# Performance work log

Hardware: AMD Instinct MI355X
Metric: run time of the kernel (lower is better)

The kernel has to match this reference:

```python
import jax, jax.numpy as jnp
import numpy as np

NUM_HEADS = 16
NUM_KV_HEADS = 8
HEAD_DIM = 128
HIDDEN = 2048
Q_SIZE = NUM_HEADS * HEAD_DIM          # 2048
KV_SIZE = NUM_KV_HEADS * HEAD_DIM      # 1024
SCALING = 256.0 ** -0.5                # query_pre_attn_scalar ** -0.5
EPS = 1e-6
BATCH = 8
ENC_LEN = 512                          # encoder_len_per_req
Q_LEN = 2048                           # sum of extend_seq_lens (8 * 256)
KV_LEN = BATCH * ENC_LEN               # 4096


def _rms_norm(x, w):
    # Gemma3RMSNorm: fp32 compute, scale by (1 + weight)
    xf = x.astype(jnp.float32)
    xf = xf * jax.lax.rsqrt(jnp.mean(xf * xf, axis=-1, keepdims=True) + EPS)
    return (xf * (1.0 + w.astype(jnp.float32))).astype(x.dtype)


def setup_inputs() -> dict:
    key = jax.random.key(0)
    k1, k2, k3 = jax.random.split(key, 3)
    return {
        "hidden_states": jax.random.normal(k1, (Q_LEN, HIDDEN), jnp.float32),
        "encoder_hidden_states": jax.random.normal(k2, (KV_LEN, HIDDEN), jnp.float32),
        "w_qkv": jax.random.normal(k3, (Q_SIZE + 2 * KV_SIZE, HIDDEN), jnp.float32) * 0.02,
        "q_norm_w": jnp.zeros((HEAD_DIM,), jnp.float32),
        "k_norm_w": jnp.zeros((HEAD_DIM,), jnp.float32),
        "seq_lens": jnp.full((BATCH,), Q_LEN // BATCH, jnp.int32),  # extend_seq_lens per request
    }


def reference(hidden_states, encoder_hidden_states, w_qkv, q_norm_w, k_norm_w, seq_lens):
    # decoder side: only q is used
    qkv_dec = hidden_states @ w_qkv.T                     # [q_len, 4096]
    q = qkv_dec[:, :Q_SIZE].reshape(Q_LEN, NUM_HEADS, HEAD_DIM)
    q = _rms_norm(q, q_norm_w) * SCALING

    # encoder side: only k, v are used
    qkv_enc = encoder_hidden_states @ w_qkv.T             # [kv_len, 4096]
    k = qkv_enc[:, Q_SIZE:Q_SIZE + KV_SIZE].reshape(KV_LEN, NUM_KV_HEADS, HEAD_DIM)
    v = qkv_enc[:, Q_SIZE + KV_SIZE:].reshape(KV_LEN, NUM_KV_HEADS, HEAD_DIM)
    k = _rms_norm(k, k_norm_w)

    # GQA: repeat each kv head n_rep times (consecutively, matching expand+reshape)
    n_rep = NUM_HEADS // NUM_KV_HEADS
    k = jnp.repeat(k, n_rep, axis=1)                      # [kv_len, H, D]
    v = jnp.repeat(v, n_rep, axis=1)

    # scores per head: [H, q_len, kv_len]
    scores = jnp.einsum('qhd,khd->hqk', q, k)

    # ragged block-diagonal mask: query token i belongs to request r iff
    # cumsum(seq_lens)[r-1] <= i < cumsum(seq_lens)[r]; kv token j -> j // ENC_LEN
    q_req = jnp.searchsorted(jnp.cumsum(seq_lens), jnp.arange(Q_LEN), side='right')
    kv_req = jnp.arange(KV_LEN) // ENC_LEN
    mask = q_req[:, None] == kv_req[None, :]              # [q_len, kv_len] bool
    scores = jnp.where(mask[None, :, :], scores, -jnp.inf)

    attn = jax.nn.softmax(scores.astype(jnp.float32), axis=-1).astype(v.dtype)
    out = jnp.einsum('hqk,khd->qhd', attn, v)             # [q_len, H, D]
    return out.reshape(Q_LEN, NUM_HEADS * HEAD_DIM)
```

## Files before the change

kernel.cpp:

```cpp
#include <hip/hip_runtime.h>

typedef __attribute__((ext_vector_type(8))) short short8;
typedef __attribute__((ext_vector_type(4))) float f32x4;

#define DEVI __device__ __forceinline__

static constexpr int HIDDEN   = 2048;
static constexpr int NHEADS   = 16;
static constexpr int NKV      = 8;
static constexpr int HDIM     = 128;
static constexpr int QLEN     = 2048;
static constexpr int KVLEN    = 4096;
static constexpr int ENCLEN   = 512;
static constexpr int NREQ     = 8;
static constexpr float SCALING = 0.0625f;
static constexpr float EPS     = 1e-6f;

DEVI unsigned short f2bf(float f) {
  unsigned int b = __float_as_uint(f);
  b += 0x7FFFu + ((b >> 16) & 1u);
  return (unsigned short)(b >> 16);
}

DEVI void g2l16(const void* g, void* l) {
  __builtin_amdgcn_global_load_lds(
      (const __attribute__((address_space(1))) void*)g,
      (__attribute__((address_space(3))) void*)l, 16, 0, 0);
}

__global__ __launch_bounds__(256) void cvt_all(const float* __restrict__ h,
                                               const float* __restrict__ e,
                                               const float* __restrict__ w,
                                               unsigned short* __restrict__ hb,
                                               unsigned short* __restrict__ eb,
                                               unsigned short* __restrict__ wb) {
  constexpr long S1 = (long)2048 * 2048, S2 = (long)4096 * 2048;
  long i = ((long)blockIdx.x * 256 + threadIdx.x) * 8;
  const float* src;
  unsigned short* dst;
  if (i < S1)           { src = h + i;            dst = hb + i; }
  else if (i < S1 + S2) { src = e + (i - S1);     dst = eb + (i - S1); }
  else                  { src = w + (i - S1 - S2); dst = wb + (i - S1 - S2); }
  float4 a = *(const float4*)src;
  float4 b = *(const float4*)(src + 4);
  short8 o;
  o[0] = (short)f2bf(a.x); o[1] = (short)f2bf(a.y);
  o[2] = (short)f2bf(a.z); o[3] = (short)f2bf(a.w);
  o[4] = (short)f2bf(b.x); o[5] = (short)f2bf(b.y);
  o[6] = (short)f2bf(b.z); o[7] = (short)f2bf(b.w);
  *(short8*)dst = o;
}


#define SBAR  __builtin_amdgcn_s_barrier()

DEVI short8 rdfrag(const char* half, int row, int g) {
  return *(const short8*)(half + row * 128 + ((g ^ (row & 7)) << 4));
}

__global__ __launch_bounds__(512, 2) void gemm_qkv8(
    const unsigned short* __restrict__ Adec, const unsigned short* __restrict__ Aenc,
    const unsigned short* __restrict__ Bw,
    const float* __restrict__ q_nw, const float* __restrict__ k_nw,
    unsigned short* __restrict__ q_bf, unsigned short* __restrict__ k_bf,
    unsigned short* __restrict__ v_t) {
  extern __shared__ char lds[];
  const int K = 2048, NKT = 32;

  int flat = blockIdx.y * 8 + blockIdx.x;
  int swz = (flat & 7) * 24 + (flat >> 3);
  int bx = swz & 7, by = swz >> 3;

  const unsigned short* A;
  int bm0;
  if (by < 8) { A = Adec; bm0 = by * 256; }
  else        { A = Aenc; bm0 = (by - 8) * 256; }
  const unsigned short* Bp = Bw + (by < 8 ? 0 : (size_t)2048 * 2048);
  const int bn0 = bx * 256;

  const int tid = threadIdx.x, lane = tid & 63, wave = tid >> 6;
  const int lr = lane & 15, lg = lane >> 4;
  const int wr = wave >> 2, wc = wave & 3;
  const int bcol0 = (wc & 1) * 64;

#define AH(b, h) (lds + (b) * 65536 + (h) * 16384)
#define BH(b, h) (lds + (b) * 65536 + 32768 + (h) * 16384)

  int srow[2], scol[2];
#pragma unroll
  for (int i = 0; i < 2; ++i) {
    int c = i * 512 + tid;
    srow[i] = c >> 3;
    scol[i] = ((c & 7) ^ ((c >> 3) & 7)) * 8;
  }

#define STG_KT(kt)                                                            \
  {                                                                           \
    const int b_ = (kt) & 1;                                                  \
    const size_t kb_ = (size_t)(kt) * 64;                                     \
    _Pragma("unroll") for (int i = 0; i < 2; ++i) {                           \
      const int d_ = (i * 512 + tid) * 16;                                    \
      g2l16(A  + (size_t)(bm0 + srow[i]) * K + kb_ + scol[i],       AH(b_, 0) + d_); \
      g2l16(A  + (size_t)(bm0 + 128 + srow[i]) * K + kb_ + scol[i], AH(b_, 1) + d_); \
      g2l16(Bp + (size_t)(bn0 + srow[i]) * K + kb_ + scol[i],       BH(b_, 0) + d_); \
      g2l16(Bp + (size_t)(bn0 + 128 + srow[i]) * K + kb_ + scol[i], BH(b_, 1) + d_); \
    }                                                                         \
  }

  f32x4 acc[8][4] = {};
  short8 a[4][2], b[2][2];

#define LOAD_A(buf, qm)                                                       \
  {                                                                           \
    const char* ah = AH(buf, wr);                                             \
    _Pragma("unroll") for (int m = 0; m < 4; ++m)                             \
        _Pragma("unroll") for (int kk = 0; kk < 2; ++kk)                      \
            a[m][kk] = rdfrag(ah, (qm) * 64 + m * 16 + lr, kk * 4 + lg);      \
  }
#define LOAD_B(buf, qn)                                                       \
  {                                                                           \
    const char* bh = BH(buf, wc >> 1);                                        \
    _Pragma("unroll") for (int n = 0; n < 2; ++n)                             \
        _Pragma("unroll") for (int kk = 0; kk < 2; ++kk)                      \
            b[n][kk] = rdfrag(bh, bcol0 + (qn) * 32 + n * 16 + lr, kk * 4 + lg); \
  }
#define MM16(qm, qn)                                                          \
  {                                                                           \
    __builtin_amdgcn_s_setprio(1);                                            \
    _Pragma("unroll") for (int m = 0; m < 4; ++m)                             \
        _Pragma("unroll") for (int n = 0; n < 2; ++n)                         \
            _Pragma("unroll") for (int kk = 0; kk < 2; ++kk)                  \
                acc[(qm)*4 + m][(qn)*2 + n] =                                 \
                    __builtin_amdgcn_mfma_f32_16x16x32_bf16(                  \
                        a[m][kk], b[n][kk], acc[(qm)*4 + m][(qn)*2 + n], 0, 0, 0); \
    __builtin_amdgcn_s_setprio(0);                                            \
  }

  STG_KT(0);
  asm volatile("s_waitcnt vmcnt(0)" ::: "memory");
  SBAR;

#pragma unroll 2
  for (int kt = 0; kt < NKT; ++kt) {
    const int cb = kt & 1;
    if (kt + 1 < NKT) STG_KT(kt + 1);
    LOAD_A(cb, 0); LOAD_B(cb, 0); SBAR; MM16(0, 0); SBAR;
    LOAD_B(cb, 1);                SBAR; MM16(0, 1); SBAR;
    LOAD_A(cb, 1); LOAD_B(cb, 0); SBAR; MM16(1, 0); SBAR;
    LOAD_B(cb, 1);                SBAR; MM16(1, 1);
    if (kt + 1 < NKT) asm volatile("s_waitcnt vmcnt(0)" ::: "memory");
    SBAR;
  }

  const int btype = (by < 8) ? 0 : (bx < 4 ? 1 : 2);
  const int tokbase0 = (by < 8 ? by : by - 8) * 256;

  if (btype < 2) {
    float* Lf = (float*)lds;
    const float* wnorm = (btype == 0) ? q_nw : k_nw;
    const float fscale = (btype == 0) ? SCALING : 1.0f;
    unsigned short* dst = (btype == 0) ? q_bf : k_bf;
    const size_t LEN = (btype == 0) ? (size_t)QLEN : (size_t)KVLEN;
    const int dloc = lr * 8;
    float wv[8];
#pragma unroll
    for (int j = 0; j < 8; ++j) wv[j] = 1.0f + wnorm[dloc + j];

#pragma unroll
    for (int q = 0; q < 4; ++q) {
      SBAR;
      if (wr == (q >> 1)) {
        const int amb = (q & 1) * 4;
#pragma unroll
        for (int am2 = 0; am2 < 4; ++am2)
#pragma unroll
          for (int n = 0; n < 4; ++n)
#pragma unroll
            for (int r = 0; r < 4; ++r)
              Lf[(am2 * 16 + lg * 4 + r) * 260 + wc * 64 + n * 16 + lr] =
                  acc[amb + am2][n][r];
      }
      SBAR;
#pragma unroll
      for (int it = 0; it < 4; ++it) {
        int pair = it * 32 + wave * 4 + (lane >> 4);
        int row = pair >> 1, hh = pair & 1;
        const float* src = &Lf[row * 260 + hh * 128 + dloc];
        f32x4 x0 = *(const f32x4*)src;
        f32x4 x1 = *(const f32x4*)(src + 4);
        float ssq = x0[0]*x0[0] + x0[1]*x0[1] + x0[2]*x0[2] + x0[3]*x0[3] +
                    x1[0]*x1[0] + x1[1]*x1[1] + x1[2]*x1[2] + x1[3]*x1[3];
#pragma unroll
        for (int m = 8; m >= 1; m >>= 1) ssq += __shfl_xor(ssq, m);
        float sc = rsqrtf(ssq * (1.0f / 128.0f) + EPS) * fscale;
        short8 o;
        o[0] = (short)f2bf(x0[0] * sc * wv[0]); o[1] = (short)f2bf(x0[1] * sc * wv[1]);
        o[2] = (short)f2bf(x0[2] * sc * wv[2]); o[3] = (short)f2bf(x0[3] * sc * wv[3]);
        o[4] = (short)f2bf(x1[0] * sc * wv[4]); o[5] = (short)f2bf(x1[1] * sc * wv[5]);
        o[6] = (short)f2bf(x1[2] * sc * wv[6]); o[7] = (short)f2bf(x1[3] * sc * wv[7]);
        int tok = tokbase0 + q * 64 + row;
        int hd = 2 * bx + hh;
        *(short8*)&dst[((size_t)hd * LEN + tok) * 128 + dloc] = o;
      }
    }
  } else {
    float* Lv = (float*)lds;
#pragma unroll
    for (int q = 0; q < 4; ++q) {
      SBAR;
      if (wr == (q >> 1)) {
        const int amb = (q & 1) * 4;
#pragma unroll
        for (int am2 = 0; am2 < 4; ++am2)
#pragma unroll
          for (int n = 0; n < 4; ++n)
            *(f32x4*)&Lv[(wc * 64 + n * 16 + lr) * 68 + am2 * 16 + lg * 4] =
                acc[amb + am2][n];
      }
      SBAR;
      int d = tid >> 1, th = tid & 1;
      const float* src = &Lv[d * 68 + th * 32];
      int kh = (bx - 4) * 2 + (d >> 7);
      int tok = tokbase0 + q * 64 + th * 32;
      unsigned short* vp = &v_t[((size_t)kh * 128 + (d & 127)) * KVLEN + tok];
#pragma unroll
      for (int j = 0; j < 4; ++j) {
        f32x4 v0 = *(const f32x4*)(src + j * 8);
        f32x4 v1 = *(const f32x4*)(src + j * 8 + 4);
        short8 o;
        o[0] = (short)f2bf(v0[0]); o[1] = (short)f2bf(v0[1]);
        o[2] = (short)f2bf(v0[2]); o[3] = (short)f2bf(v0[3]);
        o[4] = (short)f2bf(v1[0]); o[5] = (short)f2bf(v1[1]);
        o[6] = (short)f2bf(v1[2]); o[7] = (short)f2bf(v1[3]);
        *(short8*)(vp + j * 8) = o;
      }
    }
  }
#undef AH
#undef BH
#undef STG_KT
#undef LOAD_A
#undef LOAD_B
#undef MM16
}

__global__ __launch_bounds__(256, 4) void attn_kernel(
    const unsigned short* __restrict__ qb,
    const unsigned short* __restrict__ kb,
    const unsigned short* __restrict__ vt,
    const int* __restrict__ seq_lens,
    float* __restrict__ out) {
  __shared__ __align__(16) char smem[73728];

  const int h = blockIdx.y;
  const int t0 = blockIdx.x * 64;
  int req = 0, qs = 0;
#pragma unroll 1
  while (req < NREQ - 1 && qs + seq_lens[req] <= t0) { qs += seq_lens[req]; ++req; }
  const int slen = seq_lens[req];
  const int rows = min(64, qs + slen - t0);
  if (rows <= 0) return;
  const int qbase = t0;

  const int tid = threadIdx.x, lane = tid & 63, wave = tid >> 6;
  const int lr = lane & 15, lg = lane >> 4;
  const int m0w = wave * 16;
  const int kh = h >> 1;
  const int kv0 = req * ENCLEN;

#define STAGE_K(c, db)                                                        \
  _Pragma("unroll") for (int i = 0; i < 4; ++i) {                             \
    int idx = i * 256 + tid;                                                  \
    int row = idx >> 4, slot = idx & 15;                                      \
    g2l16(kb + ((size_t)kh * KVLEN + kv0 + (c) * 64 + row) * 128 +            \
              ((slot ^ (row & 15)) << 3),                                     \
          smem + (db) * 16384 + idx * 16);                                    \
  }
#define STAGE_V(c, db)                                                        \
  _Pragma("unroll") for (int i = 0; i < 4; ++i) {                             \
    int idx = i * 256 + tid;                                                  \
    int row = idx >> 3, slot = idx & 7;                                       \
    g2l16(vt + ((size_t)kh * 128 + row) * KVLEN + kv0 + (c) * 64 +            \
              ((slot ^ (row & 7)) << 3),                                      \
          smem + 32768 + (db) * 16384 + idx * 16);                            \
  }

  unsigned short* Ps = (unsigned short*)(smem + 65536);

  short8 a_q[4];
  {
    int qr = qbase + min(m0w + lr, rows - 1);
    const unsigned short* qp = qb + ((size_t)h * QLEN + qr) * 128 + lg * 8;
#pragma unroll
    for (int ks = 0; ks < 4; ++ks) a_q[ks] = *(const short8*)(qp + ks * 32);
  }

  f32x4 acc[8] = {};
  float mrow[4], lsum[4];
#pragma unroll
  for (int r = 0; r < 4; ++r) { mrow[r] = -1e30f; lsum[r] = 0.f; }

  STAGE_K(0, 0); STAGE_V(0, 0);

  int cb = 0;
#pragma unroll 1
  for (int c = 0; c < 8; ++c) {
    asm volatile("s_waitcnt vmcnt(0)" ::: "memory");
    __syncthreads();
    if (c < 7) { STAGE_K(c + 1, cb ^ 1); STAGE_V(c + 1, cb ^ 1); }
    const unsigned short* Kb = (const unsigned short*)(smem + cb * 16384);
    const unsigned short* Vb = (const unsigned short*)(smem + 32768 + cb * 16384);

    f32x4 s[4] = {};
#pragma unroll
    for (int ks = 0; ks < 4; ++ks) {
      short8 bk[4];
#pragma unroll
      for (int n = 0; n < 4; ++n) {
        int row = n * 16 + lr;
        bk[n] = *(const short8*)&Kb[row * 128 + (((ks * 4 + lg) ^ (row & 15)) << 3)];
      }
#pragma unroll
      for (int n = 0; n < 4; ++n)
        s[n] = __builtin_amdgcn_mfma_f32_16x16x32_bf16(a_q[ks], bk[n], s[n], 0, 0, 0);
    }

#pragma unroll
    for (int r = 0; r < 4; ++r) {
      float mx = fmaxf(fmaxf(s[0][r], s[1][r]), fmaxf(s[2][r], s[3][r]));
#pragma unroll
      for (int msk = 8; msk >= 1; msk >>= 1) mx = fmaxf(mx, __shfl_xor(mx, msk));
      float mnew = fmaxf(mrow[r], mx);
      float al = __expf(mrow[r] - mnew);
      mrow[r] = mnew;
      float rs = 0.f;
#pragma unroll
      for (int n = 0; n < 4; ++n) {
        float p = __expf(s[n][r] - mnew);
        s[n][r] = p;
        rs += p;
      }
#pragma unroll
      for (int msk = 8; msk >= 1; msk >>= 1) rs += __shfl_xor(rs, msk);
      lsum[r] = lsum[r] * al + rs;
#pragma unroll
      for (int n2 = 0; n2 < 8; ++n2) acc[n2][r] *= al;
    }

#pragma unroll
    for (int n = 0; n < 4; ++n)
#pragma unroll
      for (int r = 0; r < 4; ++r) {
        int row = m0w + lg * 4 + r;
        int col = n * 16 + lr;
        Ps[row * 64 + (col ^ ((row & 7) << 3))] = f2bf(s[n][r]);
      }
    asm volatile("s_waitcnt lgkmcnt(0)" ::: "memory");
    __builtin_amdgcn_sched_barrier(0);

#pragma unroll
    for (int ks = 0; ks < 2; ++ks) {
      int prow = m0w + lr;
      short8 pa = *(const short8*)&Ps[prow * 64 + (((ks * 4 + lg) ^ (prow & 7)) << 3)];
#pragma unroll
      for (int n2 = 0; n2 < 8; ++n2) {
        int row = n2 * 16 + lr;
        short8 bv = *(const short8*)&Vb[row * 64 + (((ks * 4 + lg) ^ (row & 7)) << 3)];
        acc[n2] = __builtin_amdgcn_mfma_f32_16x16x32_bf16(pa, bv, acc[n2], 0, 0, 0);
      }
    }
    cb ^= 1;
  }
  __syncthreads();

  float inv[4];
#pragma unroll
  for (int r = 0; r < 4; ++r) inv[r] = 1.0f / lsum[r];
#pragma unroll
  for (int n2 = 0; n2 < 8; ++n2)
#pragma unroll
    for (int r = 0; r < 4; ++r) acc[n2][r] *= inv[r];

  constexpr int OFS = 132;
  float* Of = (float*)smem;
#pragma unroll
  for (int n2 = 0; n2 < 8; ++n2)
#pragma unroll
    for (int r = 0; r < 4; ++r)
      Of[(m0w + lg * 4 + r) * OFS + n2 * 16 + lr] = acc[n2][r];
  __syncthreads();
#pragma unroll
  for (int p = 0; p < 8; ++p) {
    int idx = p * 256 + tid;
    int row = idx >> 5, c4 = (idx & 31) * 4;
    if (row < rows) {
      f32x4 v = *(const f32x4*)&Of[row * OFS + c4];
      *(f32x4*)&out[(size_t)(qbase + row) * 2048 + h * 128 + c4] = v;
    }
  }
#undef STAGE_K
#undef STAGE_V
}

extern "C" void kernel_launch(void* const* d_in, const int* in_sizes, int n_in,
                              void* d_out, int out_size, void* d_ws, size_t ws_size,
                              hipStream_t stream) {
  const float* hidden = (const float*)d_in[0];
  const float* enc    = (const float*)d_in[1];
  const float* w_qkv  = (const float*)d_in[2];
  const float* q_nw   = (const float*)d_in[3];
  const float* k_nw   = (const float*)d_in[4];
  const int*   slens  = (const int*)d_in[5];
  float* out = (float*)d_out;

  char* ws = (char*)d_ws;
  unsigned short* h_bf = (unsigned short*)(ws + 0);
  unsigned short* e_bf = (unsigned short*)(ws + 8388608);
  unsigned short* w_bf = (unsigned short*)(ws + 25165824);
  unsigned short* q_bf = (unsigned short*)(ws + 41943040);
  unsigned short* k_bf = (unsigned short*)(ws + 50331648);
  unsigned short* v_t  = (unsigned short*)(ws + 58720256);

  static bool attr_set = false;
  if (!attr_set) {
    hipFuncSetAttribute((const void*)gemm_qkv8,
                        hipFuncAttributeMaxDynamicSharedMemorySize, 131072);
    attr_set = true;
  }

  cvt_all<<<10240, 256, 0, stream>>>(hidden, enc, w_qkv, h_bf, e_bf, w_bf);

  gemm_qkv8<<<dim3(8, 24), 512, 131072, stream>>>(h_bf, e_bf, w_bf, q_nw, k_nw,
                                                  q_bf, k_bf, v_t);

  attn_kernel<<<dim3(32, 16), 256, 0, stream>>>(q_bf, k_bf, v_t, slens, out);
}
```

Before: 114.4 us.

## Interleave half-tile global staging with MFMA phases in QKV GEMM main loop

The QKV projection GEMM main loop is restructured. Global-to-LDS staging is split into half-tile A and B chunks, spread across four compute phases per k-tile, and B is prefetched one tile further ahead than A. Each wave now loads its B fragments once per k-tile and its A fragments per quarter, and waits on global loads with a partial vmcnt instead of draining fully each iteration. The goal is to overlap memory traffic with MFMA work and cut full-drain stalls, at the cost of more barriers and more complex hand scheduling.

```diff
diff --git a/kernel.cpp b/kernel.cpp
--- a/kernel.cpp
+++ b/kernel.cpp
@@ -65,7 +65,7 @@
     unsigned short* __restrict__ q_bf, unsigned short* __restrict__ k_bf,
     unsigned short* __restrict__ v_t) {
   extern __shared__ char lds[];
-  const int K = 2048, NKT = 32;
+  const int K = 2048;
 
   int flat = blockIdx.y * 8 + blockIdx.x;
   int swz = (flat & 7) * 24 + (flat >> 3);
@@ -81,75 +81,87 @@
   const int tid = threadIdx.x, lane = tid & 63, wave = tid >> 6;
   const int lr = lane & 15, lg = lane >> 4;
   const int wr = wave >> 2, wc = wave & 3;
-  const int bcol0 = (wc & 1) * 64;
-
-#define AH(b, h) (lds + (b) * 65536 + (h) * 16384)
-#define BH(b, h) (lds + (b) * 65536 + 32768 + (h) * 16384)
 
   int srow[2], scol[2];
 #pragma unroll
-  for (int i = 0; i < 2; ++i) {
-    int c = i * 512 + tid;
-    srow[i] = c >> 3;
-    scol[i] = ((c & 7) ^ ((c >> 3) & 7)) * 8;
-  }
-
-#define STG_KT(kt)                                                            \
-  {                                                                           \
-    const int b_ = (kt) & 1;                                                  \
-    const size_t kb_ = (size_t)(kt) * 64;                                     \
-    _Pragma("unroll") for (int i = 0; i < 2; ++i) {                           \
-      const int d_ = (i * 512 + tid) * 16;                                    \
-      g2l16(A  + (size_t)(bm0 + srow[i]) * K + kb_ + scol[i],       AH(b_, 0) + d_); \
-      g2l16(A  + (size_t)(bm0 + 128 + srow[i]) * K + kb_ + scol[i], AH(b_, 1) + d_); \
-      g2l16(Bp + (size_t)(bn0 + srow[i]) * K + kb_ + scol[i],       BH(b_, 0) + d_); \
-      g2l16(Bp + (size_t)(bn0 + 128 + srow[i]) * K + kb_ + scol[i], BH(b_, 1) + d_); \
-    }                                                                         \
-  }
+  for (int i2 = 0; i2 < 2; ++i2) {
+    int c = i2 * 512 + tid;
+    srow[i2] = c >> 3;
+    scol[i2] = ((c & 7) ^ ((c >> 3) & 7)) * 8;
+  }
+
+#define STGH_A(kt, h)                                                         \
+  { _Pragma("unroll") for (int i2 = 0; i2 < 2; ++i2)                          \
+      g2l16(A + (size_t)(bm0 + (h) * 128 + srow[i2]) * K + (size_t)(kt) * 64 + scol[i2], \
+            lds + (((kt) & 1) << 16) + ((h) << 14) + (i2 * 512 + tid) * 16); }
+#define STGH_B(kt, h)                                                         \
+  { _Pragma("unroll") for (int i2 = 0; i2 < 2; ++i2)                          \
+      g2l16(Bp + (size_t)(bn0 + (h) * 128 + srow[i2]) * K + (size_t)(kt) * 64 + scol[i2], \
+            lds + (((kt) & 1) << 16) + 32768 + ((h) << 14) + (i2 * 512 + tid) * 16); }
 
   f32x4 acc[8][4] = {};
-  short8 a[4][2], b[2][2];
-
-#define LOAD_A(buf, qm)                                                       \
-  {                                                                           \
-    const char* ah = AH(buf, wr);                                             \
-    _Pragma("unroll") for (int m = 0; m < 4; ++m)                             \
+  short8 a[2][2], b[4][2];
+
+#define RDB(buf)                                                              \
+  { const char* bh = lds + ((buf) << 16) + 32768 + ((wc >> 1) << 14);         \
+    _Pragma("unroll") for (int n = 0; n < 4; ++n)                             \
+      _Pragma("unroll") for (int kk = 0; kk < 2; ++kk)                        \
+        b[n][kk] = rdfrag(bh, (wc & 1) * 64 + n * 16 + lr, kk * 4 + lg); }
+#define RDA(buf, q)                                                           \
+  { const char* ah = lds + ((buf) << 16) + (wr << 14);                        \
+    _Pragma("unroll") for (int j = 0; j < 2; ++j)                             \
+      _Pragma("unroll") for (int kk = 0; kk < 2; ++kk)                        \
+        a[j][kk] = rdfrag(ah, ((q) * 2 + j) * 16 + lr, kk * 4 + lg); }
+#define MM16(q)                                                               \
+  { __builtin_amdgcn_s_setprio(1);                                            \
+    _Pragma("unroll") for (int j = 0; j < 2; ++j)                             \
+      _Pragma("unroll") for (int n = 0; n < 4; ++n)                           \
         _Pragma("unroll") for (int kk = 0; kk < 2; ++kk)                      \
-            a[m][kk] = rdfrag(ah, (qm) * 64 + m * 16 + lr, kk * 4 + lg);      \
-  }
-#define LOAD_B(buf, qn)                                                       \
-  {                                                                           \
-    const char* bh = BH(buf, wc >> 1);                                        \
-    _Pragma("unroll") for (int n = 0; n < 2; ++n)                             \
-        _Pragma("unroll") for (int kk = 0; kk < 2; ++kk)                      \
-            b[n][kk] = rdfrag(bh, bcol0 + (qn) * 32 + n * 16 + lr, kk * 4 + lg); \
-  }
-#define MM16(qm, qn)                                                          \
-  {                                                                           \
-    __builtin_amdgcn_s_setprio(1);                                            \
-    _Pragma("unroll") for (int m = 0; m < 4; ++m)                             \
-        _Pragma("unroll") for (int n = 0; n < 2; ++n)                         \
-            _Pragma("unroll") for (int kk = 0; kk < 2; ++kk)                  \
-                acc[(qm)*4 + m][(qn)*2 + n] =                                 \
-                    __builtin_amdgcn_mfma_f32_16x16x32_bf16(                  \
-                        a[m][kk], b[n][kk], acc[(qm)*4 + m][(qn)*2 + n], 0, 0, 0); \
-    __builtin_amdgcn_s_setprio(0);                                            \
-  }
-
-  STG_KT(0);
-  asm volatile("s_waitcnt vmcnt(0)" ::: "memory");
-  SBAR;
-
-#pragma unroll 2
-  for (int kt = 0; kt < NKT; ++kt) {
-    const int cb = kt & 1;
-    if (kt + 1 < NKT) STG_KT(kt + 1);
-    LOAD_A(cb, 0); LOAD_B(cb, 0); SBAR; MM16(0, 0); SBAR;
-    LOAD_B(cb, 1);                SBAR; MM16(0, 1); SBAR;
-    LOAD_A(cb, 1); LOAD_B(cb, 0); SBAR; MM16(1, 0); SBAR;
-    LOAD_B(cb, 1);                SBAR; MM16(1, 1);
-    if (kt + 1 < NKT) asm volatile("s_waitcnt vmcnt(0)" ::: "memory");
-    SBAR;
+          acc[(q) * 2 + j][n] = __builtin_amdgcn_mfma_f32_16x16x32_bf16(      \
+              a[j][kk], b[n][kk], acc[(q) * 2 + j][n], 0, 0, 0);              \
+    __builtin_amdgcn_s_setprio(0); }
+
+#define VM4 asm volatile("s_waitcnt vmcnt(4)" ::: "memory")
+#define VM0 asm volatile("s_waitcnt vmcnt(0)" ::: "memory")
+#define NOPS ((void)0)
+
+#define PH(q, buf, VM_STMT, STG_STMT)                                         \
+  { VM_STMT;                                                                  \
+    if ((q) == 0) RDB(buf);                                                   \
+    RDA(buf, q);                                                              \
+    STG_STMT;                                                                 \
+    SBAR;                                                                     \
+    asm volatile("s_waitcnt lgkmcnt(0)" ::: "memory");                        \
+    __builtin_amdgcn_sched_barrier(0);                                        \
+    MM16(q);                                                                  \
+    SBAR; }
+
+  STGH_A(0, 0); STGH_A(0, 1);
+  STGH_B(0, 0); STGH_B(0, 1);
+  STGH_B(1, 0); STGH_B(1, 1);
+  VM0; SBAR;
+
+#pragma unroll 1
+  for (int i = 0; i < 15; ++i) {
+    const int k1 = 2 * i + 1, k2 = 2 * i + 2, k3 = 2 * i + 3;
+    PH(0, 0, VM4,  STGH_A(k1, 0));
+    PH(1, 0, NOPS, STGH_A(k1, 1));
+    PH(2, 0, NOPS, STGH_B(k2, 0));
+    PH(3, 0, NOPS, STGH_B(k2, 1));
+    PH(0, 1, VM4,  STGH_A(k2, 0));
+    PH(1, 1, NOPS, STGH_A(k2, 1));
+    PH(2, 1, NOPS, STGH_B(k3, 0));
+    PH(3, 1, NOPS, STGH_B(k3, 1));
+  }
+  {
+    PH(0, 0, VM4,  STGH_A(31, 0));
+    PH(1, 0, NOPS, STGH_A(31, 1));
+    PH(2, 0, NOPS, NOPS);
+    PH(3, 0, NOPS, NOPS);
+    PH(0, 1, VM0,  NOPS);
+    PH(1, 1, NOPS, NOPS);
+    PH(2, 1, NOPS, NOPS);
+    PH(3, 1, NOPS, NOPS);
   }
 
   const int btype = (by < 8) ? 0 : (bx < 4 ? 1 : 2);
@@ -236,12 +248,15 @@
       }
     }
   }
-#undef AH
-#undef BH
-#undef STG_KT
-#undef LOAD_A
-#undef LOAD_B
+#undef STGH_A
+#undef STGH_B
+#undef RDB
+#undef RDA
 #undef MM16
+#undef VM4
+#undef VM0
+#undef NOPS
+#undef PH
 }
 
 __global__ __launch_bounds__(256, 4) void attn_kernel(
```

New measurement: 104.6 us. 8.6% less time.
